# Performance work log

Hardware: AMD Instinct MI355X
Metric: run time of the kernel (lower is better)

The kernel has to match this reference:

```python
import jax, jax.numpy as jnp
import numpy as np

B, L, C, H, W = 4, 5, 64, 128, 256
VOXEL = 0.4          # args['voxel_size'][0]
DOWNSAMPLE = 2       # args['downsample_rate']


def setup_inputs() -> dict:
    key = jax.random.key(0)
    k1, k2, k3 = jax.random.split(key, 3)
    record_len = jnp.array([3, 5, 4, 4], dtype=jnp.int32)  # sum = 16
    n_tot = 16
    x = jax.random.normal(k1, (n_tot, C, H, W), dtype=jnp.float32)
    # near-identity SE(2)-ish 4x4 transforms so warps stay mostly in-bounds
    eye = jnp.eye(4, dtype=jnp.float32)
    t = jnp.broadcast_to(eye, (B, L, L, 4, 4)).copy()
    rot = jax.random.normal(k2, (B, L, L, 2, 2), dtype=jnp.float32) * 0.02
    trans = jax.random.normal(k3, (B, L, L, 2), dtype=jnp.float32) * 5.0  # meters
    t = t.at[..., :2, :2].add(rot)
    t = t.at[..., 0, 3].set(trans[..., 0])
    t = t.at[..., 1, 3].set(trans[..., 1])
    return {"x": x, "record_len": record_len, "pairwise_t_matrix": t}


def _normalize_t(t):
    # t: (B,L,L,4,4) -> normalized 2x3 affine (matches the torch in-place edits)
    m = t[..., jnp.array([0, 1]), :][..., jnp.array([0, 1, 3])]  # (B,L,L,2,3)
    m = m.at[..., 0, 1].multiply(H / W)
    m = m.at[..., 1, 0].multiply(W / H)
    m = m.at[..., 0, 2].multiply(2.0 / (DOWNSAMPLE * VOXEL * W))
    m = m.at[..., 1, 2].multiply(2.0 / (DOWNSAMPLE * VOXEL * H))
    return m


def _grid_sample(img, grid):
    # img (N,C,H,W), grid (N,H,W,2) xy in [-1,1]; bilinear, zeros padding,
    # align_corners=True (matches torch warp_affine_simple / F.grid_sample)
    n, c, h, w = img.shape
    ix = (grid[..., 0] + 1.0) * 0.5 * (w - 1)
    iy = (grid[..., 1] + 1.0) * 0.5 * (h - 1)
    x0 = jnp.floor(ix); y0 = jnp.floor(iy)
    x1 = x0 + 1.0;      y1 = y0 + 1.0
    wx1 = ix - x0; wx0 = 1.0 - wx1
    wy1 = iy - y0; wy0 = 1.0 - wy1

    def corner(xc, yc, wgt):
        valid = (xc >= 0) & (xc <= w - 1) & (yc >= 0) & (yc <= h - 1)
        xi = jnp.clip(xc, 0, w - 1).astype(jnp.int32)
        yi = jnp.clip(yc, 0, h - 1).astype(jnp.int32)
        vals = jax.vmap(lambda im, yy, xx: im[:, yy, xx])(img, yi, xi)  # (N,C,H,W)
        return vals * (wgt * valid)[:, None, :, :]

    return (corner(x0, y0, wx0 * wy0) + corner(x1, y0, wx1 * wy0)
            + corner(x0, y1, wx0 * wy1) + corner(x1, y1, wx1 * wy1))


def _fuse(x, record_len, pairwise_t_matrix):
    m = _normalize_t(pairwise_t_matrix)          # (B,L,L,2,3)
    theta = m[:, 0]                              # ego row i=0 -> (B,L,2,3)
    # affine_grid, align_corners=True: base grid over [-1,1]
    xs = jnp.linspace(-1.0, 1.0, W)
    ys = jnp.linspace(-1.0, 1.0, H)
    gx, gy = jnp.meshgrid(xs, ys)                # (H,W)
    coords = jnp.stack([gx, gy, jnp.ones_like(gx)], axis=-1)  # (H,W,3)
    grid = jnp.einsum('blij,hwj->blhwi', theta, coords)        # (B,L,H,W,2)
    # pad ragged groups to (B,L,...) via gather
    csum = jnp.cumsum(record_len)
    offsets = jnp.concatenate([jnp.zeros((1,), csum.dtype), csum[:-1]])
    idx = jnp.clip(offsets[:, None] + jnp.arange(L)[None, :], 0, x.shape[0] - 1)
    xp = x[idx]                                  # (B,L,C,H,W)
    warped = _grid_sample(xp.reshape(B * L, C, H, W),
                          grid.reshape(B * L, H, W, 2)).reshape(B, L, C, H, W)
    mask = jnp.arange(L)[None, :] < record_len[:, None]        # (B,L)
    neg_inf = jnp.array(-jnp.inf, dtype=warped.dtype)
    masked = jnp.where(mask[:, :, None, None, None], warped, neg_inf)
    return jnp.max(masked, axis=1)               # (B,C,H,W)


def reference(x, record_len, pairwise_t_matrix):
    return _fuse(x, record_len, pairwise_t_matrix)
```

## Files before the change

### kernel.cpp

```cpp
#include <hip/hip_runtime.h>
#include <math.h>

#define BB 4
#define LL 5
#define CC 64
#define HH 128
#define WW 256
#define NTOT 16
#define CG 8
#define HW (HH * WW)
#define NWG (BB * (CC / CG) * HH)

__global__ __launch_bounds__(256) void maxfusion_kernel(
    const float* __restrict__ x,
    const int* __restrict__ record_len,
    const float* __restrict__ t,
    float* __restrict__ out)
{
    const int cg  = blockIdx.x % 8;
    const int idx = blockIdx.x / 8;
    const int h   = idx % HH;
    const int b   = idx / HH;
    const int w   = threadIdx.x;

    const int rl = record_len[b];
    int off = 0;
    #pragma unroll
    for (int j = 0; j < BB; ++j) off += (j < b) ? record_len[j] : 0;

    const float gx = -1.0f + 2.0f * (float)w / (float)(WW - 1);
    const float gy = -1.0f + 2.0f * (float)h / (float)(HH - 1);

    float maxv[CG];
    #pragma unroll
    for (int c = 0; c < CG; ++c) maxv[c] = -INFINITY;

    for (int l = 0; l < rl; ++l) {
        const float* tm = t + (size_t)((b * LL * LL + l) * 16);
        const float m00 = tm[0];
        const float m01 = tm[1] * ((float)HH / (float)WW);
        const float m02 = tm[3] * (2.0f / (0.8f * (float)WW));
        const float m10 = tm[4] * ((float)WW / (float)HH);
        const float m11 = tm[5];
        const float m12 = tm[7] * (2.0f / (0.8f * (float)HH));
        const float sx  = 0.5f * (float)(WW - 1);
        const float sy  = 0.5f * (float)(HH - 1);
        const float a00 = m00 * sx, a01 = m01 * sx, a02 = (m02 + 1.0f) * sx;
        const float a10 = m10 * sy, a11 = m11 * sy, a12 = (m12 + 1.0f) * sy;

        const float ix = a00 * gx + a01 * gy + a02;
        const float iy = a10 * gx + a11 * gy + a12;

        const float x0f = floorf(ix), y0f = floorf(iy);
        const float wx1 = ix - x0f, wx0 = 1.0f - wx1;
        const float wy1 = iy - y0f, wy0 = 1.0f - wy1;
        const int x0 = (int)x0f, y0 = (int)y0f;

        const bool inx = (x0 >= 0) && (x0 <= WW - 2);
        const float wxa = inx ? wx0 : ((x0 == -1)     ? wx1 : 0.0f);
        const float wxb = inx ? wx1 : ((x0 == WW - 1) ? wx0 : 0.0f);
        const float wy0v = ((y0 >= 0)     && (y0 <= HH - 1))     ? wy0 : 0.0f;
        const float wy1v = ((y0 + 1 >= 0) && (y0 + 1 <= HH - 1)) ? wy1 : 0.0f;

        const int k  = min(max(x0, 0), WW - 2);
        const int r0 = min(max(y0,     0), HH - 1);
        const int r1 = min(max(y0 + 1, 0), HH - 1);
        const int off0 = r0 * WW + k;
        const int off1 = r1 * WW + k;

        const int n = off + l;
        const float* base = x + ((size_t)n * CC + (size_t)cg * CG) * HW;

        #pragma unroll
        for (int c = 0; c < CG; ++c) {
            const float* p = base + (size_t)c * HW;
            const float2 q0 = *reinterpret_cast<const float2*>(p + off0);
            const float2 q1 = *reinterpret_cast<const float2*>(p + off1);
            const float t0 = q0.x * wxa + q0.y * wxb;
            const float t1 = q1.x * wxa + q1.y * wxb;
            const float v  = t0 * wy0v + t1 * wy1v;
            maxv[c] = fmaxf(maxv[c], v);
        }
    }

    float* ob = out + (((size_t)b * CC + (size_t)cg * CG) * HH + h) * WW + w;
    #pragma unroll
    for (int c = 0; c < CG; ++c)
        __builtin_nontemporal_store(maxv[c], ob + (size_t)c * HW);
}

extern "C" void kernel_launch(void* const* d_in, const int* in_sizes, int n_in,
                              void* d_out, int out_size, void* d_ws, size_t ws_size,
                              hipStream_t stream) {
    const float* x          = (const float*)d_in[0];
    const int*   record_len = (const int*)d_in[1];
    const float* t          = (const float*)d_in[2];
    float* out = (float*)d_out;

    maxfusion_kernel<<<NWG, 256, 0, stream>>>(x, record_len, t, out);
}
```

Measured before the change: 40.74 us.

## Stage warped row band in LDS per channel and row-block for bilinear sampling

Each workgroup now handles one channel and a block of 8 output rows. For every input agent it loads a 16-row band of the source image into shared memory with coalesced float4 loads. Bilinear taps are then read from LDS, with a global-memory fallback for lanes whose source rows fall outside the band. This replaces scattered global float2 gathers with coalesced staging and reuse across rows. In exchange it adds two barriers per agent, 16 KB of LDS per block, and extra loaded rows that may go unused.

Result: slower. 46.69 us (+14.6%).

```diff
diff --git a/kernel.cpp b/kernel.cpp
--- a/kernel.cpp
+++ b/kernel.cpp
@@ -7,9 +7,11 @@
 #define HH 128
 #define WW 256
 #define NTOT 16
-#define CG 8
+#define HB 8
+#define BAND 16
 #define HW (HH * WW)
-#define NWG (BB * (CC / CG) * HH)
+#define NHB (HH / HB)
+#define NWG (BB * CC * NHB)
 
 __global__ __launch_bounds__(256) void maxfusion_kernel(
     const float* __restrict__ x,
@@ -17,11 +19,17 @@
     const float* __restrict__ t,
     float* __restrict__ out)
 {
-    const int cg  = blockIdx.x % 8;
-    const int idx = blockIdx.x / 8;
-    const int h   = idx % HH;
-    const int b   = idx / HH;
-    const int w   = threadIdx.x;
+    __shared__ float lds[BAND * WW];
+
+    const int c_lo  = blockIdx.x & 7;
+    const int inner = blockIdx.x >> 3;
+    const int hb    = inner & (NHB - 1);
+    const int c_hi  = (inner >> 4) & 7;
+    const int b     = inner >> 7;
+    const int c     = c_lo + 8 * c_hi;
+    const int h0    = hb * HB;
+    const int tid   = threadIdx.x;
+    const int w     = tid;
 
     const int rl = record_len[b];
     int off = 0;
@@ -29,11 +37,10 @@
     for (int j = 0; j < BB; ++j) off += (j < b) ? record_len[j] : 0;
 
     const float gx = -1.0f + 2.0f * (float)w / (float)(WW - 1);
-    const float gy = -1.0f + 2.0f * (float)h / (float)(HH - 1);
 
-    float maxv[CG];
+    float maxv[HB];
     #pragma unroll
-    for (int c = 0; c < CG; ++c) maxv[c] = -INFINITY;
+    for (int hh = 0; hh < HB; ++hh) maxv[hh] = -INFINITY;
 
     for (int l = 0; l < rl; ++l) {
         const float* tm = t + (size_t)((b * LL * LL + l) * 16);
@@ -48,45 +55,74 @@
         const float a00 = m00 * sx, a01 = m01 * sx, a02 = (m02 + 1.0f) * sx;
         const float a10 = m10 * sy, a11 = m11 * sy, a12 = (m12 + 1.0f) * sy;
 
-        const float ix = a00 * gx + a01 * gy + a02;
-        const float iy = a10 * gx + a11 * gy + a12;
+        const float gy0 = -1.0f + 2.0f * (float)h0 / (float)(HH - 1);
+        const float gy1 = -1.0f + 2.0f * (float)(h0 + HB - 1) / (float)(HH - 1);
+        const float iyA = -a10 + a11 * gy0 + a12;
+        const float iyB =  a10 + a11 * gy0 + a12;
+        const float iyC = -a10 + a11 * gy1 + a12;
+        const float iyD =  a10 + a11 * gy1 + a12;
+        const int ymin = (int)floorf(fminf(fminf(iyA, iyB), fminf(iyC, iyD)));
 
-        const float x0f = floorf(ix), y0f = floorf(iy);
-        const float wx1 = ix - x0f, wx0 = 1.0f - wx1;
-        const float wy1 = iy - y0f, wy0 = 1.0f - wy1;
-        const int x0 = (int)x0f, y0 = (int)y0f;
+        const float* base = x + ((size_t)(off + l) * CC + c) * HW;
 
-        const bool inx = (x0 >= 0) && (x0 <= WW - 2);
-        const float wxa = inx ? wx0 : ((x0 == -1)     ? wx1 : 0.0f);
-        const float wxb = inx ? wx1 : ((x0 == WW - 1) ? wx0 : 0.0f);
-        const float wy0v = ((y0 >= 0)     && (y0 <= HH - 1))     ? wy0 : 0.0f;
-        const float wy1v = ((y0 + 1 >= 0) && (y0 + 1 <= HH - 1)) ? wy1 : 0.0f;
-
-        const int k  = min(max(x0, 0), WW - 2);
-        const int r0 = min(max(y0,     0), HH - 1);
-        const int r1 = min(max(y0 + 1, 0), HH - 1);
-        const int off0 = r0 * WW + k;
-        const int off1 = r1 * WW + k;
-
-        const int n = off + l;
-        const float* base = x + ((size_t)n * CC + (size_t)cg * CG) * HW;
+        __syncthreads();
+        #pragma unroll
+        for (int r = 0; r < 4; ++r) {
+            const int flat  = r * 256 + tid;
+            const int j     = flat >> 6;
+            const int chunk = flat & 63;
+            const int rr    = min(max(ymin + j, 0), HH - 1);
+            const float4 v  = *reinterpret_cast<const float4*>(
+                                  base + (size_t)rr * WW + chunk * 4);
+            *reinterpret_cast<float4*>(&lds[j * WW + chunk * 4]) = v;
+        }
+        __syncthreads();
 
         #pragma unroll
-        for (int c = 0; c < CG; ++c) {
-            const float* p = base + (size_t)c * HW;
-            const float2 q0 = *reinterpret_cast<const float2*>(p + off0);
-            const float2 q1 = *reinterpret_cast<const float2*>(p + off1);
-            const float t0 = q0.x * wxa + q0.y * wxb;
-            const float t1 = q1.x * wxa + q1.y * wxb;
-            const float v  = t0 * wy0v + t1 * wy1v;
-            maxv[c] = fmaxf(maxv[c], v);
+        for (int hh = 0; hh < HB; ++hh) {
+            const float gy = -1.0f + 2.0f * (float)(h0 + hh) / (float)(HH - 1);
+            const float ix = a00 * gx + a01 * gy + a02;
+            const float iy = a10 * gx + a11 * gy + a12;
+
+            const float x0f = floorf(ix), y0f = floorf(iy);
+            const float wx1 = ix - x0f, wx0 = 1.0f - wx1;
+            const float wy1 = iy - y0f, wy0 = 1.0f - wy1;
+            const int x0 = (int)x0f, y0 = (int)y0f;
+
+            const bool inx = (x0 >= 0) && (x0 <= WW - 2);
+            const float wxa  = inx ? wx0 : ((x0 == -1)     ? wx1 : 0.0f);
+            const float wxb  = inx ? wx1 : ((x0 == WW - 1) ? wx0 : 0.0f);
+            const float wy0v = ((y0 >= 0)     && (y0 <= HH - 1))     ? wy0 : 0.0f;
+            const float wy1v = ((y0 + 1 >= 0) && (y0 + 1 <= HH - 1)) ? wy1 : 0.0f;
+
+            const int k = min(max(x0, 0), WW - 2);
+
+            const int slot   = y0 - ymin;
+            const bool inband = (slot >= 0) && (slot <= BAND - 2);
+            const int slotc  = min(max(slot, 0), BAND - 2);
+
+            float2 v0 = *reinterpret_cast<const float2*>(&lds[slotc * WW + k]);
+            float2 v1 = *reinterpret_cast<const float2*>(&lds[slotc * WW + WW + k]);
+
+            if (__any(!inband)) {
+                if (!inband) {
+                    const int r0c = min(max(y0,     0), HH - 1);
+                    const int r1c = min(max(y0 + 1, 0), HH - 1);
+                    v0 = *reinterpret_cast<const float2*>(base + (size_t)r0c * WW + k);
+                    v1 = *reinterpret_cast<const float2*>(base + (size_t)r1c * WW + k);
+                }
+            }
+
+            const float t0 = v0.x * wxa + v0.y * wxb;
+            const float t1 = v1.x * wxa + v1.y * wxb;
+            maxv[hh] = fmaxf(maxv[hh], t0 * wy0v + t1 * wy1v);
         }
     }
 
-    float* ob = out + (((size_t)b * CC + (size_t)cg * CG) * HH + h) * WW + w;
+    float* ob = out + (((size_t)b * CC + c) * HH + h0) * WW + w;
     #pragma unroll
-    for (int c = 0; c < CG; ++c)
-        __builtin_nontemporal_store(maxv[c], ob + (size_t)c * HW);
+    for (int hh = 0; hh < HB; ++hh)
+        __builtin_nontemporal_store(maxv[hh], ob + (size_t)hh * WW);
 }
 
 extern "C" void kernel_launch(void* const* d_in, const int* in_sizes, int n_in,
```
